# Kernel tuning notes

Hardware: AMD Instinct MI355X
Metric: run time of the kernel (lower is better)

## Reference

```python
import jax, jax.numpy as jnp
import numpy as np

IN_DIM, HID_DIM, OUT_DIM = 128, 128, 10
NUM_NODE, NUM_EDGE = 16384, 524288


def setup_inputs() -> dict:
    key = jax.random.key(0)
    ks = jax.random.split(key, 12)
    N = NUM_NODE
    fts = jax.random.normal(ks[0], (N, IN_DIM), dtype=jnp.float32)
    edge_index = jax.random.randint(ks[1], (2, NUM_EDGE), 0, N, dtype=jnp.int64)
    def lin(k, fan_in, fan_out):
        bound = 1.0 / np.sqrt(fan_in)
        k1, k2 = jax.random.split(k)
        W = jax.random.uniform(k1, (fan_in, fan_out), jnp.float32, -bound, bound)
        b = jax.random.uniform(k2, (fan_out,), jnp.float32, -bound, bound)
        return W, b
    W_mlp0, b_mlp0 = lin(ks[2], N, 128)
    W_mlp1, b_mlp1 = lin(ks[3], 128, 128)
    W_g1, b_g1 = lin(ks[4], IN_DIM, HID_DIM)
    W_g2, b_g2 = lin(ks[5], HID_DIM, HID_DIM)
    W_c, b_c = lin(ks[6], HID_DIM, OUT_DIM)
    return {"fts": fts, "edge_index": edge_index,
            "W_mlp0": W_mlp0, "b_mlp0": b_mlp0, "W_mlp1": W_mlp1, "b_mlp1": b_mlp1,
            "W_g1": W_g1, "b_g1": b_g1, "W_g2": W_g2, "b_g2": b_g2,
            "W_c": W_c, "b_c": b_c, "num_node": NUM_NODE}


def _gcn_conv(x, W, b, row, col, n):
    # PyG GCNConv: x W, then sym-normalized aggregation over edges+self-loops, then +b
    x = x @ W
    deg = jax.ops.segment_sum(jnp.ones(row.shape[0], x.dtype), col, num_segments=n)
    dinv = jnp.where(deg > 0, jax.lax.rsqrt(jnp.maximum(deg, 1e-12)), 0.0)
    norm = dinv[row] * dinv[col]                      # [E+N]
    out = jax.ops.segment_sum(x[row] * norm[:, None], col, num_segments=n)
    return out + b


def reference(fts, edge_index, W_mlp0, b_mlp0, W_mlp1, b_mlp1,
              W_g1, b_g1, W_g2, b_g2, W_c, b_c, num_node):
    n = num_node
    row, col = edge_index[0], edge_index[1]
    # dense adjacency scatter-set (faithful to torch code; result feeds the MLP branch)
    adj = jnp.zeros((n, n), jnp.float32).at[row, col].set(1.0)
    adj = jax.nn.relu(adj @ W_mlp0 + b_mlp0)
    adj = jax.nn.relu(adj @ W_mlp1 + b_mlp1)          # computed but unused downstream, as in source
    # edges with self-loops for GCNConv
    loops = jnp.arange(n, dtype=row.dtype)
    r = jnp.concatenate([row, loops])
    c = jnp.concatenate([col, loops])
    x = jax.nn.relu(_gcn_conv(fts, W_g1, b_g1, r, c, n))   # dropout is identity in eval mode
    x = jax.nn.relu(_gcn_conv(x, W_g2, b_g2, r, c, n))
    out = x @ W_c + b_c
    return (out, x)
```

## Files before the change

### kernel.cpp

```cpp
#include <hip/hip_runtime.h>


#define NNODE 16384
#define NEDGE 524288
#define DIM   128
#define CAP   128

__device__ __forceinline__ float bflo(unsigned u) { return __uint_as_float(u << 16); }
__device__ __forceinline__ float bfhi(unsigned u) { return __uint_as_float(u & 0xFFFF0000u); }
__device__ __forceinline__ unsigned f2bf(float x) {
    unsigned u = __float_as_uint(x);
    return (u + 0x7FFFu + ((u >> 16) & 1u)) >> 16;
}

__global__ __launch_bounds__(256) void k_zero(int* __restrict__ p) {
    p[blockIdx.x * 256 + threadIdx.x] = 0;
}

__global__ __launch_bounds__(256) void k_fill(const int* __restrict__ erow,
                                              const int* __restrict__ ecol,
                                              int* __restrict__ cnt,
                                              int* __restrict__ nbr) {
    int e = blockIdx.x * 256 + threadIdx.x;
    int r = erow[e] & (NNODE - 1);
    int c = ecol[e] & (NNODE - 1);
    int pos = atomicAdd(&cnt[c], 1) & (CAP - 1);
    nbr[(c << 7) + pos] = r;
}

__global__ __launch_bounds__(256) void k_dinv(const int* __restrict__ cnt,
                                              float* __restrict__ dinv) {
    int i = blockIdx.x * 256 + threadIdx.x;
    dinv[i] = rsqrtf((float)(cnt[i] + 1));
}

__global__ __launch_bounds__(256) void k_gemm_scale(
    const float* __restrict__ A, const float* __restrict__ W,
    const float* __restrict__ dinv, unsigned short* __restrict__ lin)
{
    __shared__ float As[128][68];
    const int tid  = threadIdx.x;
    const int row0 = blockIdx.x * 64;
    const int col0 = blockIdx.y * 64;

    #pragma unroll
    for (int it = 0; it < 32; ++it) {
        int idx = it * 256 + tid;
        int r = idx >> 7, k = idx & 127;
        As[k][r] = A[(row0 + r) * DIM + k];
    }
    __syncthreads();

    const int tx = tid & 15, ty = tid >> 4;
    float acc[4][4] = {{0.f}};

    #pragma unroll 8
    for (int k = 0; k < 128; ++k) {
        float4 a = *(const float4*)&As[k][ty * 4];
        float4 w = *(const float4*)&W[k * DIM + col0 + tx * 4];
        acc[0][0] += a.x * w.x; acc[0][1] += a.x * w.y; acc[0][2] += a.x * w.z; acc[0][3] += a.x * w.w;
        acc[1][0] += a.y * w.x; acc[1][1] += a.y * w.y; acc[1][2] += a.y * w.z; acc[1][3] += a.y * w.w;
        acc[2][0] += a.z * w.x; acc[2][1] += a.z * w.y; acc[2][2] += a.z * w.z; acc[2][3] += a.z * w.w;
        acc[3][0] += a.w * w.x; acc[3][1] += a.w * w.y; acc[3][2] += a.w * w.z; acc[3][3] += a.w * w.w;
    }

    #pragma unroll
    for (int i = 0; i < 4; ++i) {
        int r = row0 + ty * 4 + i;
        float s = dinv[r];
        unsigned p0 = f2bf(acc[i][0] * s) | (f2bf(acc[i][1] * s) << 16);
        unsigned p1 = f2bf(acc[i][2] * s) | (f2bf(acc[i][3] * s) << 16);
        *(uint2*)&lin[r * DIM + col0 + tx * 4] = make_uint2(p0, p1);
    }
}

template<bool FINAL>
__global__ __launch_bounds__(256) void k_gather(
    const int* __restrict__ cnt, const int* __restrict__ nbr,
    const unsigned short* __restrict__ lin, const float* __restrict__ dinv,
    const float* __restrict__ bias, float* __restrict__ out,
    const float* __restrict__ Wc, const float* __restrict__ bc,
    float* __restrict__ out10)
{
    __shared__ float Ws[FINAL ? DIM * 10 : 4];
    const int tid = threadIdx.x;
    if (FINAL) {
        for (int i = tid; i < DIM * 10; i += 256) Ws[i] = Wc[i];
        __syncthreads();
    }

    const int node = blockIdx.x * 4 + (tid >> 6);
    const int lane = tid & 63;
    const int grp  = lane >> 4;
    const int cl   = lane & 15;
    const int deg  = cnt[node];
    const int nb   = node << 7;

    float a[8] = {0.f,0.f,0.f,0.f,0.f,0.f,0.f,0.f};
    if (grp == 0) {
        uint4 u = *(const uint4*)&lin[(node << 7) + cl * 8];
        a[0] = bflo(u.x); a[1] = bfhi(u.x); a[2] = bflo(u.y); a[3] = bfhi(u.y);
        a[4] = bflo(u.z); a[5] = bfhi(u.z); a[6] = bflo(u.w); a[7] = bfhi(u.w);
    }

    int i = grp;
    for (; i + 4 < deg; i += 8) {
        int r0 = nbr[nb + i];
        int r1 = nbr[nb + i + 4];
        uint4 u0 = *(const uint4*)&lin[(r0 << 7) + cl * 8];
        uint4 u1 = *(const uint4*)&lin[(r1 << 7) + cl * 8];
        a[0] += bflo(u0.x) + bflo(u1.x);  a[1] += bfhi(u0.x) + bfhi(u1.x);
        a[2] += bflo(u0.y) + bflo(u1.y);  a[3] += bfhi(u0.y) + bfhi(u1.y);
        a[4] += bflo(u0.z) + bflo(u1.z);  a[5] += bfhi(u0.z) + bfhi(u1.z);
        a[6] += bflo(u0.w) + bflo(u1.w);  a[7] += bfhi(u0.w) + bfhi(u1.w);
    }
    for (; i < deg; i += 4) {
        int r = nbr[nb + i];
        uint4 u = *(const uint4*)&lin[(r << 7) + cl * 8];
        a[0] += bflo(u.x); a[1] += bfhi(u.x); a[2] += bflo(u.y); a[3] += bfhi(u.y);
        a[4] += bflo(u.z); a[5] += bfhi(u.z); a[6] += bflo(u.w); a[7] += bfhi(u.w);
    }

    #pragma unroll
    for (int k = 0; k < 8; ++k) {
        a[k] += __shfl_xor(a[k], 16);
        a[k] += __shfl_xor(a[k], 32);
    }

    const float s = dinv[node];
    const float4 b0 = *(const float4*)&bias[cl * 8];
    const float4 b1 = *(const float4*)&bias[cl * 8 + 4];
    a[0] = fmaxf(fmaf(a[0], s, b0.x), 0.f);
    a[1] = fmaxf(fmaf(a[1], s, b0.y), 0.f);
    a[2] = fmaxf(fmaf(a[2], s, b0.z), 0.f);
    a[3] = fmaxf(fmaf(a[3], s, b0.w), 0.f);
    a[4] = fmaxf(fmaf(a[4], s, b1.x), 0.f);
    a[5] = fmaxf(fmaf(a[5], s, b1.y), 0.f);
    a[6] = fmaxf(fmaf(a[6], s, b1.z), 0.f);
    a[7] = fmaxf(fmaf(a[7], s, b1.w), 0.f);

    if (grp == 0) *(float4*)&out[node * DIM + cl * 8]     = make_float4(a[0], a[1], a[2], a[3]);
    if (grp == 1) *(float4*)&out[node * DIM + cl * 8 + 4] = make_float4(a[4], a[5], a[6], a[7]);

    if (FINAL) {
        if (grp < 2) {
            const int jb = grp * 5;
            float s0 = 0.f, s1 = 0.f, s2 = 0.f, s3 = 0.f, s4 = 0.f;
            #pragma unroll
            for (int u = 0; u < 8; ++u) {
                const float xv = a[u];
                const float* wrow = &Ws[(cl * 8 + u) * 10 + jb];
                s0 = fmaf(xv, wrow[0], s0);
                s1 = fmaf(xv, wrow[1], s1);
                s2 = fmaf(xv, wrow[2], s2);
                s3 = fmaf(xv, wrow[3], s3);
                s4 = fmaf(xv, wrow[4], s4);
            }
            #pragma unroll
            for (int off = 1; off < 16; off <<= 1) {
                s0 += __shfl_xor(s0, off);
                s1 += __shfl_xor(s1, off);
                s2 += __shfl_xor(s2, off);
                s3 += __shfl_xor(s3, off);
                s4 += __shfl_xor(s4, off);
            }
            if (cl == 0) {
                float* o = &out10[node * 10 + jb];
                o[0] = s0 + bc[jb + 0];
                o[1] = s1 + bc[jb + 1];
                o[2] = s2 + bc[jb + 2];
                o[3] = s3 + bc[jb + 3];
                o[4] = s4 + bc[jb + 4];
            }
        }
    }
}

extern "C" void kernel_launch(void* const* d_in, const int* in_sizes, int n_in,
                              void* d_out, int out_size, void* d_ws, size_t ws_size,
                              hipStream_t stream)
{
    const float* fts  = (const float*)d_in[0];
    const int*   erow = (const int*)d_in[1];
    const int*   ecol = erow + NEDGE;
    const float* W_g1 = (const float*)d_in[6];
    const float* b_g1 = (const float*)d_in[7];
    const float* W_g2 = (const float*)d_in[8];
    const float* b_g2 = (const float*)d_in[9];
    const float* W_c  = (const float*)d_in[10];
    const float* b_c  = (const float*)d_in[11];

    float* out  = (float*)d_out;
    float* xout = out + NNODE * 10;

    float*          dinv  = (float*)d_ws;
    int*            cnt   = (int*)(dinv + NNODE);
    int*            nbr   = cnt + NNODE;
    float*          bufB  = (float*)(nbr + NNODE * CAP);
    unsigned short* lin16 = (unsigned short*)(bufB + NNODE * DIM);

    k_zero<<<NNODE / 256, 256, 0, stream>>>(cnt);
    k_fill<<<NEDGE / 256, 256, 0, stream>>>(erow, ecol, cnt, nbr);
    k_dinv<<<NNODE / 256, 256, 0, stream>>>(cnt, dinv);

    k_gemm_scale<<<dim3(NNODE / 64, 2), 256, 0, stream>>>(fts, W_g1, dinv, lin16);
    k_gather<false><<<NNODE / 4, 256, 0, stream>>>(cnt, nbr, lin16, dinv, b_g1, bufB,
                                                   nullptr, nullptr, nullptr);
    k_gemm_scale<<<dim3(NNODE / 64, 2), 256, 0, stream>>>(bufB, W_g2, dinv, lin16);
    k_gather<true><<<NNODE / 4, 256, 0, stream>>>(cnt, nbr, lin16, dinv, b_g2, xout,
                                                  W_c, b_c, out);
}
```

Before: 185.4 us.

## Shrink neighbor list to uint16, fuse dinv into consumers, unroll gather deeper

Neighbor indices are stored as 16-bit values instead of 32-bit, which halves the adjacency list traffic. The separate zero and dinv kernels are dropped: the zeroing becomes a hipMemsetAsync and rsqrt(deg+1) is computed inline in the GEMM and gather kernels. The gather loop is unrolled to four neighbor loads per iteration to keep more loads in flight. The cost is a few extra rsqrt computations and mask operations per node.

```diff
diff --git a/kernel.cpp b/kernel.cpp
--- a/kernel.cpp
+++ b/kernel.cpp
@@ -5,6 +5,7 @@
 #define NEDGE 524288
 #define DIM   128
 #define CAP   128
+#define NMASK (NNODE - 1)
 
 __device__ __forceinline__ float bflo(unsigned u) { return __uint_as_float(u << 16); }
 __device__ __forceinline__ float bfhi(unsigned u) { return __uint_as_float(u & 0xFFFF0000u); }
@@ -13,30 +14,20 @@
     return (u + 0x7FFFu + ((u >> 16) & 1u)) >> 16;
 }
 
-__global__ __launch_bounds__(256) void k_zero(int* __restrict__ p) {
-    p[blockIdx.x * 256 + threadIdx.x] = 0;
-}
-
 __global__ __launch_bounds__(256) void k_fill(const int* __restrict__ erow,
                                               const int* __restrict__ ecol,
                                               int* __restrict__ cnt,
-                                              int* __restrict__ nbr) {
+                                              unsigned short* __restrict__ nbr) {
     int e = blockIdx.x * 256 + threadIdx.x;
-    int r = erow[e] & (NNODE - 1);
-    int c = ecol[e] & (NNODE - 1);
+    int r = erow[e] & NMASK;
+    int c = ecol[e] & NMASK;
     int pos = atomicAdd(&cnt[c], 1) & (CAP - 1);
-    nbr[(c << 7) + pos] = r;
-}
-
-__global__ __launch_bounds__(256) void k_dinv(const int* __restrict__ cnt,
-                                              float* __restrict__ dinv) {
-    int i = blockIdx.x * 256 + threadIdx.x;
-    dinv[i] = rsqrtf((float)(cnt[i] + 1));
+    nbr[(c << 7) + pos] = (unsigned short)r;
 }
 
 __global__ __launch_bounds__(256) void k_gemm_scale(
     const float* __restrict__ A, const float* __restrict__ W,
-    const float* __restrict__ dinv, unsigned short* __restrict__ lin)
+    const int* __restrict__ cnt, unsigned short* __restrict__ lin)
 {
     __shared__ float As[128][68];
     const int tid  = threadIdx.x;
@@ -67,7 +58,7 @@
     #pragma unroll
     for (int i = 0; i < 4; ++i) {
         int r = row0 + ty * 4 + i;
-        float s = dinv[r];
+        float s = rsqrtf((float)(cnt[r] + 1));
         unsigned p0 = f2bf(acc[i][0] * s) | (f2bf(acc[i][1] * s) << 16);
         unsigned p1 = f2bf(acc[i][2] * s) | (f2bf(acc[i][3] * s) << 16);
         *(uint2*)&lin[r * DIM + col0 + tx * 4] = make_uint2(p0, p1);
@@ -76,8 +67,8 @@
 
 template<bool FINAL>
 __global__ __launch_bounds__(256) void k_gather(
-    const int* __restrict__ cnt, const int* __restrict__ nbr,
-    const unsigned short* __restrict__ lin, const float* __restrict__ dinv,
+    const int* __restrict__ cnt, const unsigned short* __restrict__ nbr,
+    const unsigned short* __restrict__ lin,
     const float* __restrict__ bias, float* __restrict__ out,
     const float* __restrict__ Wc, const float* __restrict__ bc,
     float* __restrict__ out10)
@@ -94,7 +85,8 @@
     const int grp  = lane >> 4;
     const int cl   = lane & 15;
     const int deg  = cnt[node];
-    const int nb   = node << 7;
+    const float dn = rsqrtf((float)(deg + 1));
+    const int  nb  = node << 7;
 
     float a[8] = {0.f,0.f,0.f,0.f,0.f,0.f,0.f,0.f};
     if (grp == 0) {
@@ -103,23 +95,30 @@
         a[4] = bflo(u.z); a[5] = bfhi(u.z); a[6] = bflo(u.w); a[7] = bfhi(u.w);
     }
 
-    int i = grp;
-    for (; i + 4 < deg; i += 8) {
-        int r0 = nbr[nb + i];
-        int r1 = nbr[nb + i + 4];
+#define ACC1(u)                                   \
+    a[0] += bflo(u.x); a[1] += bfhi(u.x);         \
+    a[2] += bflo(u.y); a[3] += bfhi(u.y);         \
+    a[4] += bflo(u.z); a[5] += bfhi(u.z);         \
+    a[6] += bflo(u.w); a[7] += bfhi(u.w);
+
+    int j = grp;
+    for (; j + 12 < deg; j += 16) {
+        int r0 = nbr[nb + j]      & NMASK;
+        int r1 = nbr[nb + j + 4]  & NMASK;
+        int r2 = nbr[nb + j + 8]  & NMASK;
+        int r3 = nbr[nb + j + 12] & NMASK;
         uint4 u0 = *(const uint4*)&lin[(r0 << 7) + cl * 8];
         uint4 u1 = *(const uint4*)&lin[(r1 << 7) + cl * 8];
-        a[0] += bflo(u0.x) + bflo(u1.x);  a[1] += bfhi(u0.x) + bfhi(u1.x);
-        a[2] += bflo(u0.y) + bflo(u1.y);  a[3] += bfhi(u0.y) + bfhi(u1.y);
-        a[4] += bflo(u0.z) + bflo(u1.z);  a[5] += bfhi(u0.z) + bfhi(u1.z);
-        a[6] += bflo(u0.w) + bflo(u1.w);  a[7] += bfhi(u0.w) + bfhi(u1.w);
-    }
-    for (; i < deg; i += 4) {
-        int r = nbr[nb + i];
+        uint4 u2 = *(const uint4*)&lin[(r2 << 7) + cl * 8];
+        uint4 u3 = *(const uint4*)&lin[(r3 << 7) + cl * 8];
+        ACC1(u0) ACC1(u1) ACC1(u2) ACC1(u3)
+    }
+    for (; j < deg; j += 4) {
+        int r = nbr[nb + j] & NMASK;
         uint4 u = *(const uint4*)&lin[(r << 7) + cl * 8];
-        a[0] += bflo(u.x); a[1] += bfhi(u.x); a[2] += bflo(u.y); a[3] += bfhi(u.y);
-        a[4] += bflo(u.z); a[5] += bfhi(u.z); a[6] += bflo(u.w); a[7] += bfhi(u.w);
-    }
+        ACC1(u)
+    }
+#undef ACC1
 
     #pragma unroll
     for (int k = 0; k < 8; ++k) {
@@ -127,17 +126,16 @@
         a[k] += __shfl_xor(a[k], 32);
     }
 
-    const float s = dinv[node];
     const float4 b0 = *(const float4*)&bias[cl * 8];
     const float4 b1 = *(const float4*)&bias[cl * 8 + 4];
-    a[0] = fmaxf(fmaf(a[0], s, b0.x), 0.f);
-    a[1] = fmaxf(fmaf(a[1], s, b0.y), 0.f);
-    a[2] = fmaxf(fmaf(a[2], s, b0.z), 0.f);
-    a[3] = fmaxf(fmaf(a[3], s, b0.w), 0.f);
-    a[4] = fmaxf(fmaf(a[4], s, b1.x), 0.f);
-    a[5] = fmaxf(fmaf(a[5], s, b1.y), 0.f);
-    a[6] = fmaxf(fmaf(a[6], s, b1.z), 0.f);
-    a[7] = fmaxf(fmaf(a[7], s, b1.w), 0.f);
+    a[0] = fmaxf(fmaf(a[0], dn, b0.x), 0.f);
+    a[1] = fmaxf(fmaf(a[1], dn, b0.y), 0.f);
+    a[2] = fmaxf(fmaf(a[2], dn, b0.z), 0.f);
+    a[3] = fmaxf(fmaf(a[3], dn, b0.w), 0.f);
+    a[4] = fmaxf(fmaf(a[4], dn, b1.x), 0.f);
+    a[5] = fmaxf(fmaf(a[5], dn, b1.y), 0.f);
+    a[6] = fmaxf(fmaf(a[6], dn, b1.z), 0.f);
+    a[7] = fmaxf(fmaf(a[7], dn, b1.w), 0.f);
 
     if (grp == 0) *(float4*)&out[node * DIM + cl * 8]     = make_float4(a[0], a[1], a[2], a[3]);
     if (grp == 1) *(float4*)&out[node * DIM + cl * 8 + 4] = make_float4(a[4], a[5], a[6], a[7]);
@@ -193,20 +191,18 @@
     float* out  = (float*)d_out;
     float* xout = out + NNODE * 10;
 
-    float*          dinv  = (float*)d_ws;
-    int*            cnt   = (int*)(dinv + NNODE);
-    int*            nbr   = cnt + NNODE;
-    float*          bufB  = (float*)(nbr + NNODE * CAP);
-    unsigned short* lin16 = (unsigned short*)(bufB + NNODE * DIM);
-
-    k_zero<<<NNODE / 256, 256, 0, stream>>>(cnt);
-    k_fill<<<NEDGE / 256, 256, 0, stream>>>(erow, ecol, cnt, nbr);
-    k_dinv<<<NNODE / 256, 256, 0, stream>>>(cnt, dinv);
-
-    k_gemm_scale<<<dim3(NNODE / 64, 2), 256, 0, stream>>>(fts, W_g1, dinv, lin16);
-    k_gather<false><<<NNODE / 4, 256, 0, stream>>>(cnt, nbr, lin16, dinv, b_g1, bufB,
+    int*            cnt   = (int*)d_ws;
+    unsigned short* nbr16 = (unsigned short*)(cnt + NNODE);
+    unsigned short* lin16 = nbr16 + NNODE * CAP;
+    float*          bufB  = (float*)(lin16 + NNODE * DIM);
+
+    hipMemsetAsync(cnt, 0, NNODE * sizeof(int), stream);
+    k_fill<<<NEDGE / 256, 256, 0, stream>>>(erow, ecol, cnt, nbr16);
+
+    k_gemm_scale<<<dim3(NNODE / 64, 2), 256, 0, stream>>>(fts, W_g1, cnt, lin16);
+    k_gather<false><<<NNODE / 4, 256, 0, stream>>>(cnt, nbr16, lin16, b_g1, bufB,
                                                    nullptr, nullptr, nullptr);
-    k_gemm_scale<<<dim3(NNODE / 64, 2), 256, 0, stream>>>(bufB, W_g2, dinv, lin16);
-    k_gather<true><<<NNODE / 4, 256, 0, stream>>>(cnt, nbr, lin16, dinv, b_g2, xout,
+    k_gemm_scale<<<dim3(NNODE / 64, 2), 256, 0, stream>>>(bufB, W_g2, cnt, lin16);
+    k_gather<true><<<NNODE / 4, 256, 0, stream>>>(cnt, nbr16, lin16, b_g2, xout,
                                                   W_c, b_c, out);
 }
```

Measured after the change: 183.4 us. No clear change (-1.1%).
